# Optimization experiments

Measured on AMD Instinct MI355X. Metric: run time of the kernel, lower is better.

Reference implementation:

```python
import jax, jax.numpy as jnp
import numpy as np

B, N, F, H, HEADS = 2, 256, 64, 64, 4
C = HEADS * H  # n_coefficients (coefficients_mlp is Identity => must equal n_heads*hidden)
EPS = 1e-5
INF = 1e5


def _lin(key, fan_in, fan_out, bias=True):
    k1, k2 = jax.random.split(key)
    w = jax.random.normal(k1, (fan_in, fan_out), jnp.float32) * (1.0 / np.sqrt(fan_in))
    if bias:
        b = jax.random.normal(k2, (fan_out,), jnp.float32) * 0.01
        return w, b
    return w


def setup_inputs() -> dict:
    key = jax.random.key(0)
    ks = jax.random.split(key, 16)
    inp = dict(
        h=jax.random.normal(ks[0], (B, N, F), jnp.float32),
        x=jax.random.normal(ks[1], (B, N, 3), jnp.float32),
        v=jax.random.normal(ks[2], (B, N, 3), jnp.float32),
    )
    inp['edge_w1'], inp['edge_b1'] = _lin(ks[3], 2 * F + 1, H)
    inp['edge_w2'], inp['edge_b2'] = _lin(ks[4], H, H)
    inp['sem_w'], inp['sem_b'] = _lin(ks[5], H, HEADS)
    inp['post_w1'], inp['post_b1'] = _lin(ks[6], C, H)
    inp['post_w2'], inp['post_b2'] = _lin(ks[7], H, H)
    inp['node_w1'], inp['node_b1'] = _lin(ks[8], C + H + F, H)
    inp['node_w2'], inp['node_b2'] = _lin(ks[9], H, F)
    inp['vel_w1'], inp['vel_b1'] = _lin(ks[10], F, H)
    inp['vel_w2'] = _lin(ks[11], H, 1, bias=False) * 0.001  # xavier gain=0.001 analogue
    inp['vmix_w'] = _lin(ks[12], C, 1, bias=False)[:, 0]
    inp['log_gamma'] = -jnp.log(jnp.linspace(1.0, 5.0, HEADS)).astype(jnp.float32)
    return inp


def reference(h, x, v, edge_w1, edge_b1, edge_w2, edge_b2, sem_w, sem_b,
              post_w1, post_b1, post_w2, post_b2, node_w1, node_b1,
              node_w2, node_b2, vel_w1, vel_b1, vel_w2, vmix_w, log_gamma):
    silu = jax.nn.silu
    n = h.shape[-2]
    eye = jnp.eye(n, dtype=h.dtype)[:, :, None]  # [N,N,1] diagonal mask

    # pairwise geometry: entry [i,j] = x_j - x_i
    x_minus_xt = x[..., None, :, :] - x[..., :, None, :]                # [B,N,N,3]
    x_norm = jnp.sqrt((x_minus_xt ** 2).sum(-1, keepdims=True) + EPS)   # [B,N,N,1]

    # pairwise node-feature concat (h_j, h_i) + distance -> edge MLP
    h_j = jnp.broadcast_to(h[..., None, :, :], (B, n, n, F))
    h_i = jnp.broadcast_to(h[..., :, None, :], (B, n, n, F))
    h_cat = jnp.concatenate([h_j, h_i, x_norm], axis=-1)                # [B,N,N,2F+1]
    h_e_mtx = silu(silu(h_cat @ edge_w1 + edge_b1) @ edge_w2 + edge_b2)  # [B,N,N,H]

    # euclidean attention: softmin over j of gamma*dist, diagonal masked out
    dist = (x_norm + INF * eye) * jnp.exp(log_gamma)                    # [B,N,N,heads]
    euclid_att = jax.nn.softmax(-dist, axis=-2)
    # semantic attention: LeakyReLU(0.2) logits, diagonal masked, softmax over j
    sem = jax.nn.leaky_relu(h_e_mtx @ sem_w + sem_b, 0.2) - INF * eye
    sem_att = jax.nn.softmax(sem, axis=-2)
    comb_att = jax.nn.softmax(euclid_att * sem_att, axis=-2)            # [B,N,N,heads]

    # attention-weighted edge features, flattened over (H, heads)
    h_e_att = (h_e_mtx[..., :, None] * comb_att[..., None, :]).reshape(B, n, n, C)

    # spatial attention (coefficients_mlp is Identity)
    unit = x_minus_xt / (x_norm + EPS)                                  # [B,N,N,3]
    # combinations.mean(dim=-3) without materializing [B,N,N,C,3]
    comb_sum = jnp.einsum('bijc,bijd->bicd', h_e_att, unit) / n         # [B,N,C,3]
    comb_norm = (comb_sum ** 2).sum(-1)                                 # [B,N,C]
    h_comb = silu(silu(comb_norm @ post_w1 + post_b1) @ post_w2 + post_b2)

    # delta_v = mean_j (v_mixing over C of combinations)
    delta_v = jnp.einsum('bijc,c,bijd->bid', h_e_att, vmix_w, unit) / n  # [B,N,3]

    h_agg = h_e_att.sum(axis=-2)                                        # sum over j -> [B,N,C]
    out = jnp.concatenate([h, h_agg, h_comb], axis=-1)
    out = silu(silu(out @ node_w1 + node_b1) @ node_w2 + node_b2)
    h_new = h + out                                                     # residual

    # coordinate / velocity update
    v_scale = silu(h_new @ vel_w1 + vel_b1) @ vel_w2                    # [B,N,1]
    v_new = delta_v + v_scale * v
    x_new = x + v_new
    return h_new, x_new, v_new
```

## Files before the change

kernel.cpp:

```cpp
#include <hip/hip_runtime.h>
#include <hip/hip_bf16.h>
#include <math.h>

#define EPSV 1e-5f
#define INFV 1e5f

typedef short bf16x8 __attribute__((ext_vector_type(8)));
typedef float f32x4 __attribute__((ext_vector_type(4)));

__device__ __forceinline__ float rcp_f(float x) { return __builtin_amdgcn_rcpf(x); }
__device__ __forceinline__ float silu_f(float v) { return v * rcp_f(1.0f + __expf(-v)); }

__device__ __forceinline__ unsigned short f2bf(float f) {
  unsigned int u = __float_as_uint(f);
  u = (u + 0x7fffu + ((u >> 16) & 1u)) >> 16;
  return (unsigned short)u;
}
__device__ __forceinline__ float bf2f(unsigned short h) {
  return __uint_as_float(((unsigned int)h) << 16);
}
__device__ __forceinline__ unsigned int pkbf(float a, float b) {
  float2 f2; f2.x = a; f2.y = b;
  __hip_bfloat162 t = __float22bfloat162_rn(f2);
  unsigned int u;
  __builtin_memcpy(&u, &t, 4);
  return u;
}

__device__ __forceinline__ void gemm64(const unsigned short* A_lds, const unsigned short* B_lds,
                                       int w, int l15, int quad, f32x4 acc[4][4]) {
#pragma unroll
  for (int tr = 0; tr < 4; ++tr)
#pragma unroll
    for (int tc = 0; tc < 4; ++tc)
      acc[tr][tc] = (f32x4){0.f, 0.f, 0.f, 0.f};
#pragma unroll
  for (int ms = 0; ms < 64; ms += 32) {
    bf16x8 af[4], bfr[4];
#pragma unroll
    for (int tr = 0; tr < 4; ++tr)
      af[tr] = *reinterpret_cast<const bf16x8*>(&A_lds[(64 * w + 16 * tr + l15) * 72 + ms + quad * 8]);
#pragma unroll
    for (int tc = 0; tc < 4; ++tc)
      bfr[tc] = *reinterpret_cast<const bf16x8*>(&B_lds[(16 * tc + l15) * 72 + ms + quad * 8]);
#pragma unroll
    for (int tr = 0; tr < 4; ++tr)
#pragma unroll
      for (int tc = 0; tc < 4; ++tc)
        acc[tr][tc] = __builtin_amdgcn_mfma_f32_16x16x32_bf16(af[tr], bfr[tc], acc[tr][tc], 0, 0, 0);
  }
}

__global__ __launch_bounds__(256, 2) void k_all(
    const float* __restrict__ h, const float* __restrict__ x, const float* __restrict__ v,
    const float* __restrict__ ew1, const float* __restrict__ eb1,
    const float* __restrict__ ew2, const float* __restrict__ eb2,
    const float* __restrict__ semw, const float* __restrict__ semb,
    const float* __restrict__ pw1, const float* __restrict__ pb1,
    const float* __restrict__ pw2, const float* __restrict__ pb2,
    const float* __restrict__ nw1, const float* __restrict__ nb1,
    const float* __restrict__ nw2, const float* __restrict__ nb2,
    const float* __restrict__ vw1, const float* __restrict__ vb1,
    const float* __restrict__ vw2, const float* __restrict__ vmix,
    const float* __restrict__ lgam, float* __restrict__ out) {

  __shared__ __align__(16) unsigned short TH[256 * 72];
  __shared__ __align__(16) char R0[9216];
  __shared__ __align__(16) char R1[9216];
  __shared__ __align__(16) unsigned short E3T[16 * 72];
  __shared__ __align__(16) float4 unit_l[256];
  __shared__ float w1dk[64];
  __shared__ float eb1l[64];
  __shared__ __align__(16) float bms[256];

  const int bid = blockIdx.x;
  const int b   = bid >> 8;
  const int i   = bid & 255;
  const int bi  = bid;
  const int tid = threadIdx.x;
  const int j   = tid;
  const int bj  = (b << 8) | j;

  const int w    = tid >> 6;
  const int lid  = tid & 63;
  const int l15  = lid & 15;
  const int quad = lid >> 4;

  unsigned short* E2Ta = (unsigned short*)R0;
  unsigned short* E2Tb = (unsigned short*)R1;
  float*  sd    = (float*)R0;
  float4* cat_l = (float4*)R1;
  float*  cn_l  = (float*)(R1 + 4096);
  float*  hag_l = (float*)(R1 + 5120);
  float4* scS   = (float4*)bms;
  float4* scP   = (float4*)bms + 8;
  float4* scD   = (float4*)bms + 12;
  float*  dvs   = bms + 64;

  float warm = 0.f;
  {
#pragma unroll
    for (int q = 0; q < 4; ++q) warm += pw1[(4 * tid + q) * 16];
#pragma unroll
    for (int q = 0; q < 6; ++q) warm += nw1[(6 * tid + q) * 16];
    warm += pw2[tid * 16] + nw2[tid * 16] + vw1[tid * 16];
    if (tid < 64) warm += eb2[tid] + pb1[tid] + pb2[tid] + nb1[tid] +
                          nb2[tid] + vb1[tid] + vw2[tid];
  }

  const float xi0 = x[bi * 3 + 0], xi1 = x[bi * 3 + 1], xi2 = x[bi * 3 + 2];
  const float dx = x[bj * 3 + 0] - xi0;
  const float dy = x[bj * 3 + 1] - xi1;
  const float dz = x[bj * 3 + 2] - xi2;
  const float dn = sqrtf(dx * dx + dy * dy + dz * dz + EPSV);
  const float invn = rcp_f(dn + EPSV);
  const float ux = dx * invn, uy = dy * invn, uz = dz * invn;
  unit_l[j] = make_float4(ux, uy, uz, dn);

  {
    const float4* hb4 = reinterpret_cast<const float4*>(h + (size_t)(b << 8) * 64);
#pragma unroll
    for (int q = 0; q < 16; ++q) {
      int idx = q * 256 + tid;
      float4 f4 = hb4[idx];
      int row = idx >> 4, c4 = idx & 15;
      uint2 pk;
      pk.x = pkbf(f4.x, f4.y);
      pk.y = pkbf(f4.z, f4.w);
      *reinterpret_cast<uint2*>(&TH[row * 72 + c4 * 4]) = pk;
    }
  }
#pragma unroll
  for (int q = 0; q < 16; ++q) {
    int idx = q * 256 + tid;
    E2Ta[(idx & 63) * 72 + (idx >> 6)] = f2bf(ew1[idx]);
  }
#pragma unroll
  for (int q = 0; q < 16; ++q) {
    int idx = q * 256 + tid;
    E2Tb[(idx & 63) * 72 + (idx >> 6)] = f2bf(ew2[idx]);
  }
#pragma unroll
  for (int q = 0; q < 2; ++q) {
    int idx = q * 256 + tid;
    int n = idx >> 6, kk = idx & 63;
    E3T[n * 72 + kk] = f2bf((n < 4) ? semw[kk * 4 + n] : vmix[kk * 4 + (n - 4)]);
    E3T[(8 + n) * 72 + kk] = 0;
  }
  if (tid < 64) { w1dk[tid] = ew1[128 * 64 + tid]; eb1l[tid] = eb1[tid]; }
  {
    int s = tid >> 6, k = tid & 63;
    const float* hrow = h + (size_t)bi * 64;
    float bp = 0.f;
#pragma unroll
    for (int f2 = 0; f2 < 16; ++f2) {
      int f = s * 16 + f2;
      bp += hrow[f] * ew1[(64 + f) * 64 + k];
    }
    bms[s * 64 + k] = bp;
  }
  __syncthreads();

  f32x4 acc[4][4];
  gemm64(TH, E2Ta, w, l15, quad, acc);

#pragma unroll
  for (int tc = 0; tc < 4; ++tc) {
    int kc = 16 * tc + l15;
    float wd = w1dk[kc];
    float ak = eb1l[kc] + bms[kc] + bms[64 + kc] + bms[128 + kc] + bms[192 + kc];
#pragma unroll
    for (int tr = 0; tr < 4; ++tr)
#pragma unroll
      for (int r = 0; r < 4; ++r) {
        int row = 64 * w + 16 * tr + quad * 4 + r;
        TH[row * 72 + kc] = f2bf(silu_f(acc[tr][tc][r] + ak + unit_l[row].w * wd));
      }
  }
  __syncthreads();

  gemm64(TH, E2Tb, w, l15, quad, acc);
#pragma unroll
  for (int tc = 0; tc < 4; ++tc) {
    float b2 = eb2[16 * tc + l15];
#pragma unroll
    for (int tr = 0; tr < 4; ++tr)
#pragma unroll
      for (int r = 0; r < 4; ++r) {
        int row = 64 * w + 16 * tr + quad * 4 + r;
        TH[row * 72 + 16 * tc + l15] = f2bf(silu_f(acc[tr][tc][r] + b2));
      }
  }

  f32x4 acc3[4];
#pragma unroll
  for (int tr = 0; tr < 4; ++tr) acc3[tr] = (f32x4){0.f, 0.f, 0.f, 0.f};
#pragma unroll
  for (int ms = 0; ms < 64; ms += 32) {
    bf16x8 b3 = *reinterpret_cast<const bf16x8*>(&E3T[l15 * 72 + ms + quad * 8]);
#pragma unroll
    for (int tr = 0; tr < 4; ++tr) {
      bf16x8 a3 = *reinterpret_cast<const bf16x8*>(&TH[(64 * w + 16 * tr + l15) * 72 + ms + quad * 8]);
      acc3[tr] = __builtin_amdgcn_mfma_f32_16x16x32_bf16(a3, b3, acc3[tr], 0, 0, 0);
    }
  }
  if (l15 < 8) {
#pragma unroll
    for (int tr = 0; tr < 4; ++tr)
#pragma unroll
      for (int r = 0; r < 4; ++r)
        sd[(64 * w + 16 * tr + quad * 4 + r) * 8 + l15] = acc3[tr][r];
  }

  float4 s01 = *reinterpret_cast<const float4*>(sd + j * 8);
  float4 s23 = *reinterpret_cast<const float4*>(sd + j * 8 + 4);
  float4 sbv = *reinterpret_cast<const float4*>(semb);
  const float diag = (j == i) ? INFV : 0.0f;
  float4 sl;
  sl.x = s01.x + sbv.x; sl.y = s01.y + sbv.y; sl.z = s01.z + sbv.z; sl.w = s01.w + sbv.w;
  sl.x = ((sl.x > 0.f) ? sl.x : 0.2f * sl.x) - diag;
  sl.y = ((sl.y > 0.f) ? sl.y : 0.2f * sl.y) - diag;
  sl.z = ((sl.z > 0.f) ? sl.z : 0.2f * sl.z) - diag;
  sl.w = ((sl.w > 0.f) ? sl.w : 0.2f * sl.w) - diag;

  float4 lg4 = *reinterpret_cast<const float4*>(lgam);
  const float dni = dn + diag;
  float4 e_eu = make_float4(__expf(-dni * __expf(lg4.x)), __expf(-dni * __expf(lg4.y)),
                            __expf(-dni * __expf(lg4.z)), __expf(-dni * __expf(lg4.w)));
  float4 e_sem = make_float4(__expf(sl.x), __expf(sl.y), __expf(sl.z), __expf(sl.w));

  float4 a8 = e_eu, b8 = e_sem;
#pragma unroll
  for (int off = 32; off >= 1; off >>= 1) {
    a8.x += __shfl_xor(a8.x, off); a8.y += __shfl_xor(a8.y, off);
    a8.z += __shfl_xor(a8.z, off); a8.w += __shfl_xor(a8.w, off);
    b8.x += __shfl_xor(b8.x, off); b8.y += __shfl_xor(b8.y, off);
    b8.z += __shfl_xor(b8.z, off); b8.w += __shfl_xor(b8.w, off);
  }
  if (lid == 0) { scS[w] = a8; scS[4 + w] = b8; }
  __syncthreads();
  float4 Se, Ss;
  {
    float4 r0 = scS[0], r1 = scS[1], r2 = scS[2], r3 = scS[3];
    Se = make_float4(r0.x + r1.x + r2.x + r3.x, r0.y + r1.y + r2.y + r3.y,
                     r0.z + r1.z + r2.z + r3.z, r0.w + r1.w + r2.w + r3.w);
    float4 s0 = scS[4], s1 = scS[5], s2 = scS[6], s3 = scS[7];
    Ss = make_float4(s0.x + s1.x + s2.x + s3.x, s0.y + s1.y + s2.y + s3.y,
                     s0.z + s1.z + s2.z + s3.z, s0.w + s1.w + s2.w + s3.w);
  }

  float4 p = make_float4((e_eu.x * rcp_f(Se.x)) * (e_sem.x * rcp_f(Ss.x)),
                         (e_eu.y * rcp_f(Se.y)) * (e_sem.y * rcp_f(Ss.y)),
                         (e_eu.z * rcp_f(Se.z)) * (e_sem.z * rcp_f(Ss.z)),
                         (e_eu.w * rcp_f(Se.w)) * (e_sem.w * rcp_f(Ss.w)));
  float4 ep = make_float4(__expf(p.x), __expf(p.y), __expf(p.z), __expf(p.w));
  float4 sp8 = ep;
#pragma unroll
  for (int off = 32; off >= 1; off >>= 1) {
    sp8.x += __shfl_xor(sp8.x, off); sp8.y += __shfl_xor(sp8.y, off);
    sp8.z += __shfl_xor(sp8.z, off); sp8.w += __shfl_xor(sp8.w, off);
  }
  if (lid == 0) scP[w] = sp8;
  __syncthreads();
  float4 Sp;
  {
    float4 r0 = scP[0], r1 = scP[1], r2 = scP[2], r3 = scP[3];
    Sp = make_float4(r0.x + r1.x + r2.x + r3.x, r0.y + r1.y + r2.y + r3.y,
                     r0.z + r1.z + r2.z + r3.z, r0.w + r1.w + r2.w + r3.w);
  }
  float4 catt = make_float4(ep.x * rcp_f(Sp.x), ep.y * rcp_f(Sp.y),
                            ep.z * rcp_f(Sp.z), ep.w * rcp_f(Sp.w));
  cat_l[j] = catt;

  float s = catt.x * s23.x + catt.y * s23.y + catt.z * s23.z + catt.w * s23.w;
  float dvx = s * ux, dvy = s * uy, dvz = s * uz;
#pragma unroll
  for (int off = 32; off >= 1; off >>= 1) {
    dvx += __shfl_xor(dvx, off); dvy += __shfl_xor(dvy, off); dvz += __shfl_xor(dvz, off);
  }
  if (lid == 0) scD[w] = make_float4(dvx, dvy, dvz, 0.f);
  __syncthreads();
  if (j == 0) {
    float4 r0 = scD[0], r1 = scD[1], r2 = scD[2], r3 = scD[3];
    const float inv = 1.0f / 256.0f;
    dvs[0] = (r0.x + r1.x + r2.x + r3.x) * inv;
    dvs[1] = (r0.y + r1.y + r2.y + r3.y) * inv;
    dvs[2] = (r0.z + r1.z + r2.z + r3.z) * inv;
  }

  {
    const int jg   = lid >> 2;
    const int ksub = lid & 3;
    const int kb   = 16 * w + 4 * ksub;
    float agg[4][4], ax[4][4], ay[4][4], az[4][4];
#pragma unroll
    for (int kk = 0; kk < 4; ++kk)
#pragma unroll
      for (int hd = 0; hd < 4; ++hd) {
        agg[kk][hd] = 0.f; ax[kk][hd] = 0.f; ay[kk][hd] = 0.f; az[kk][hd] = 0.f;
      }
#pragma unroll 4
    for (int jr = 0; jr < 16; ++jr) {
      int jj = jr * 16 + jg;
      ushort4 hv4 = *reinterpret_cast<const ushort4*>(&TH[jj * 72 + kb]);
      float4 ca = cat_l[jj];
      float4 u  = unit_l[jj];
      float hev[4] = { bf2f(hv4.x), bf2f(hv4.y), bf2f(hv4.z), bf2f(hv4.w) };
#pragma unroll
      for (int kk = 0; kk < 4; ++kk) {
        float c0 = hev[kk] * ca.x, c1 = hev[kk] * ca.y, c2 = hev[kk] * ca.z, c3 = hev[kk] * ca.w;
        agg[kk][0] += c0; agg[kk][1] += c1; agg[kk][2] += c2; agg[kk][3] += c3;
        ax[kk][0] += c0 * u.x; ay[kk][0] += c0 * u.y; az[kk][0] += c0 * u.z;
        ax[kk][1] += c1 * u.x; ay[kk][1] += c1 * u.y; az[kk][1] += c1 * u.z;
        ax[kk][2] += c2 * u.x; ay[kk][2] += c2 * u.y; az[kk][2] += c2 * u.z;
        ax[kk][3] += c3 * u.x; ay[kk][3] += c3 * u.y; az[kk][3] += c3 * u.z;
      }
    }
#pragma unroll
    for (int off = 4; off <= 32; off <<= 1)
#pragma unroll
      for (int kk = 0; kk < 4; ++kk)
#pragma unroll
        for (int hd = 0; hd < 4; ++hd) {
          agg[kk][hd] += __shfl_xor(agg[kk][hd], off);
          ax[kk][hd]  += __shfl_xor(ax[kk][hd], off);
          ay[kk][hd]  += __shfl_xor(ay[kk][hd], off);
          az[kk][hd]  += __shfl_xor(az[kk][hd], off);
        }
    if (jg == 0) {
      const float inv = 1.0f / 256.0f;
#pragma unroll
      for (int kk = 0; kk < 4; ++kk) {
        int k = kb + kk;
        f32x4 cnv, hgv;
#pragma unroll
        for (int hd = 0; hd < 4; ++hd) {
          float cx = ax[kk][hd] * inv, cy = ay[kk][hd] * inv, cz = az[kk][hd] * inv;
          cnv[hd] = cx * cx + cy * cy + cz * cz;
          hgv[hd] = agg[kk][hd];
        }
        *reinterpret_cast<f32x4*>(&cn_l[k * 4])  = cnv;
        *reinterpret_cast<f32x4*>(&hag_l[k * 4]) = hgv;
      }
    }
  }
  __syncthreads();

  asm volatile("" :: "v"(warm));

  {
    const int k = lid;
    float* tmpg = (float*)TH;
    float a1 = 0.f;
#pragma unroll 16
    for (int m2 = 0; m2 < 64; ++m2) {
      int m = 64 * w + m2;
      a1 += cn_l[m] * pw1[m * 64 + k];
    }
    tmpg[w * 64 + k] = a1;
    if (w == 1 || w == 2) {
      float a2 = 0.f;
      int base = (w - 1) * 128;
#pragma unroll 16
      for (int m2 = 0; m2 < 128; ++m2) {
        int m = base + m2;
        a2 += hag_l[m] * nw1[(64 + m) * 64 + k];
      }
      tmpg[256 + (w - 1) * 64 + k] = a2;
    } else if (w == 3) {
      float a2 = 0.f;
      const float* hrow = h + (size_t)bi * 64;
#pragma unroll 16
      for (int m = 0; m < 64; ++m) a2 += hrow[m] * nw1[m * 64 + k];
      tmpg[384 + k] = a2;
    }
  }
  __syncthreads();

  if (w == 0) {
    const int k = lid;
    float* tmpg = (float*)TH;
    float* sh2  = tmpg + 512;

    float m1 = silu_f(pb1[k] + tmpg[k] + tmpg[64 + k] + tmpg[128 + k] + tmpg[192 + k]);
    sh2[k] = m1;

    float a = 0.f;
#pragma unroll 16
    for (int m = 0; m < 64; ++m) a += sh2[m] * pw2[m * 64 + k];
    float hcomb = silu_f(pb2[k] + a);
    sh2[64 + k] = hcomb;

    a = nb1[k] + tmpg[256 + k] + tmpg[320 + k] + tmpg[384 + k];
#pragma unroll 16
    for (int m = 0; m < 64; ++m) a += sh2[64 + m] * nw1[(320 + m) * 64 + k];
    sh2[128 + k] = silu_f(a);

    a = 0.f;
#pragma unroll 16
    for (int m = 0; m < 64; ++m) a += sh2[128 + m] * nw2[m * 64 + k];
    float hn = h[(size_t)bi * 64 + k] + silu_f(nb2[k] + a);
    out[(size_t)bi * 64 + k] = hn;
    sh2[192 + k] = hn;

    a = 0.f;
#pragma unroll 16
    for (int m = 0; m < 64; ++m) a += sh2[192 + m] * vw1[m * 64 + k];
    float vh = silu_f(vb1[k] + a) * vw2[k];
#pragma unroll
    for (int off = 32; off >= 1; off >>= 1) vh += __shfl_xor(vh, off);

    if (k == 0) {
      const float xi[3] = {xi0, xi1, xi2};
#pragma unroll
      for (int d = 0; d < 3; ++d) {
        float vn = dvs[d] + vh * v[bi * 3 + d];
        out[32768 + bi * 3 + d] = xi[d] + vn;
        out[34304 + bi * 3 + d] = vn;
      }
    }
  }
}

extern "C" void kernel_launch(void* const* d_in, const int* in_sizes, int n_in,
                              void* d_out, int out_size, void* d_ws, size_t ws_size,
                              hipStream_t stream) {
  const float* h    = (const float*)d_in[0];
  const float* x    = (const float*)d_in[1];
  const float* v    = (const float*)d_in[2];
  const float* ew1  = (const float*)d_in[3];
  const float* eb1  = (const float*)d_in[4];
  const float* ew2  = (const float*)d_in[5];
  const float* eb2  = (const float*)d_in[6];
  const float* semw = (const float*)d_in[7];
  const float* semb = (const float*)d_in[8];
  const float* pw1  = (const float*)d_in[9];
  const float* pb1  = (const float*)d_in[10];
  const float* pw2  = (const float*)d_in[11];
  const float* pb2  = (const float*)d_in[12];
  const float* nw1  = (const float*)d_in[13];
  const float* nb1  = (const float*)d_in[14];
  const float* nw2  = (const float*)d_in[15];
  const float* nb2  = (const float*)d_in[16];
  const float* vw1  = (const float*)d_in[17];
  const float* vb1  = (const float*)d_in[18];
  const float* vw2  = (const float*)d_in[19];
  const float* vmix = (const float*)d_in[20];
  const float* lgam = (const float*)d_in[21];
  float* out = (float*)d_out;

  k_all<<<512, 256, 0, stream>>>(h, x, v, ew1, eb1, ew2, eb2, semw, semb,
                                 pw1, pb1, pw2, pb2, nw1, nb1, nw2, nb2,
                                 vw1, vb1, vw2, vmix, lgam, out);
}
```

Measured before the change: 128.6 us.

## Pre-pack bf16 weights and h in prep kernel, load MFMA B fragments into registers

Result: no change. 130.0 us (+1.1%).

```diff
diff --git a/kernel.cpp b/kernel.cpp
--- a/kernel.cpp
+++ b/kernel.cpp
@@ -19,55 +19,50 @@
 __device__ __forceinline__ float bf2f(unsigned short h) {
   return __uint_as_float(((unsigned int)h) << 16);
 }
-__device__ __forceinline__ unsigned int pkbf(float a, float b) {
-  float2 f2; f2.x = a; f2.y = b;
-  __hip_bfloat162 t = __float22bfloat162_rn(f2);
-  unsigned int u;
-  __builtin_memcpy(&u, &t, 4);
-  return u;
+
+__global__ __launch_bounds__(256) void k_prep(
+    const float* __restrict__ ew1, const float* __restrict__ ew2,
+    const float* __restrict__ semw, const float* __restrict__ vmix,
+    const float* __restrict__ h, unsigned short* __restrict__ ws16) {
+  int gid = blockIdx.x * 256 + threadIdx.x;
+  if (gid < 4096) {
+    int fi = gid >> 9, l = (gid >> 3) & 63, e = gid & 7;
+    int tc = fi >> 1, ms = fi & 1;
+    int f = ms * 32 + (l >> 4) * 8 + e, k = tc * 16 + (l & 15);
+    ws16[gid] = f2bf(ew1[f * 64 + k]);
+  } else if (gid < 8192) {
+    int t = gid - 4096;
+    int fi = t >> 9, l = (t >> 3) & 63, e = t & 7;
+    int tc = fi >> 1, ms = fi & 1;
+    int f = ms * 32 + (l >> 4) * 8 + e, k = tc * 16 + (l & 15);
+    ws16[gid] = f2bf(ew2[f * 64 + k]);
+  } else if (gid < 9216) {
+    int t = gid - 8192;
+    int fi = t >> 9, l = (t >> 3) & 63, e = t & 7;
+    int n = l & 15, kk = fi * 32 + (l >> 4) * 8 + e;
+    float v = (n < 4) ? semw[kk * 4 + n] : (n < 8 ? vmix[kk * 4 + (n - 4)] : 0.f);
+    ws16[gid] = f2bf(v);
+  } else {
+    ws16[gid] = f2bf(h[gid - 9216]);
+  }
 }
 
-__device__ __forceinline__ void gemm64(const unsigned short* A_lds, const unsigned short* B_lds,
-                                       int w, int l15, int quad, f32x4 acc[4][4]) {
-#pragma unroll
-  for (int tr = 0; tr < 4; ++tr)
-#pragma unroll
-    for (int tc = 0; tc < 4; ++tc)
-      acc[tr][tc] = (f32x4){0.f, 0.f, 0.f, 0.f};
-#pragma unroll
-  for (int ms = 0; ms < 64; ms += 32) {
-    bf16x8 af[4], bfr[4];
-#pragma unroll
-    for (int tr = 0; tr < 4; ++tr)
-      af[tr] = *reinterpret_cast<const bf16x8*>(&A_lds[(64 * w + 16 * tr + l15) * 72 + ms + quad * 8]);
-#pragma unroll
-    for (int tc = 0; tc < 4; ++tc)
-      bfr[tc] = *reinterpret_cast<const bf16x8*>(&B_lds[(16 * tc + l15) * 72 + ms + quad * 8]);
-#pragma unroll
-    for (int tr = 0; tr < 4; ++tr)
-#pragma unroll
-      for (int tc = 0; tc < 4; ++tc)
-        acc[tr][tc] = __builtin_amdgcn_mfma_f32_16x16x32_bf16(af[tr], bfr[tc], acc[tr][tc], 0, 0, 0);
-  }
-}
-
-__global__ __launch_bounds__(256, 2) void k_all(
+__global__ __launch_bounds__(256, 3) void k_all(
     const float* __restrict__ h, const float* __restrict__ x, const float* __restrict__ v,
     const float* __restrict__ ew1, const float* __restrict__ eb1,
-    const float* __restrict__ ew2, const float* __restrict__ eb2,
-    const float* __restrict__ semw, const float* __restrict__ semb,
+    const float* __restrict__ eb2,
+    const float* __restrict__ semb,
     const float* __restrict__ pw1, const float* __restrict__ pb1,
     const float* __restrict__ pw2, const float* __restrict__ pb2,
     const float* __restrict__ nw1, const float* __restrict__ nb1,
     const float* __restrict__ nw2, const float* __restrict__ nb2,
     const float* __restrict__ vw1, const float* __restrict__ vb1,
-    const float* __restrict__ vw2, const float* __restrict__ vmix,
-    const float* __restrict__ lgam, float* __restrict__ out) {
+    const float* __restrict__ vw2,
+    const float* __restrict__ lgam,
+    const unsigned short* __restrict__ wsb, float* __restrict__ out) {
 
   __shared__ __align__(16) unsigned short TH[256 * 72];
-  __shared__ __align__(16) char R0[9216];
-  __shared__ __align__(16) char R1[9216];
-  __shared__ __align__(16) unsigned short E3T[16 * 72];
+  __shared__ __align__(16) float sd[2048];
   __shared__ __align__(16) float4 unit_l[256];
   __shared__ float w1dk[64];
   __shared__ float eb1l[64];
@@ -86,12 +81,9 @@
   const int l15  = lid & 15;
   const int quad = lid >> 4;
 
-  unsigned short* E2Ta = (unsigned short*)R0;
-  unsigned short* E2Tb = (unsigned short*)R1;
-  float*  sd    = (float*)R0;
-  float4* cat_l = (float4*)R1;
-  float*  cn_l  = (float*)(R1 + 4096);
-  float*  hag_l = (float*)(R1 + 5120);
+  float4* cat_l = (float4*)sd;
+  float*  cn_l  = sd + 1024;
+  float*  hag_l = sd + 1280;
   float4* scS   = (float4*)bms;
   float4* scP   = (float4*)bms + 8;
   float4* scD   = (float4*)bms + 12;
@@ -107,6 +99,11 @@
     if (tid < 64) warm += eb2[tid] + pb1[tid] + pb2[tid] + nb1[tid] +
                           nb2[tid] + vb1[tid] + vw2[tid];
   }
+
+  bf16x8 B1f[8];
+#pragma unroll
+  for (int fi = 0; fi < 8; ++fi)
+    B1f[fi] = *reinterpret_cast<const bf16x8*>(wsb + fi * 512 + lid * 8);
 
   const float xi0 = x[bi * 3 + 0], xi1 = x[bi * 3 + 1], xi2 = x[bi * 3 + 2];
   const float dx = x[bj * 3 + 0] - xi0;
@@ -117,35 +114,11 @@
   const float ux = dx * invn, uy = dy * invn, uz = dz * invn;
   unit_l[j] = make_float4(ux, uy, uz, dn);
 
-  {
-    const float4* hb4 = reinterpret_cast<const float4*>(h + (size_t)(b << 8) * 64);
-#pragma unroll
-    for (int q = 0; q < 16; ++q) {
-      int idx = q * 256 + tid;
-      float4 f4 = hb4[idx];
-      int row = idx >> 4, c4 = idx & 15;
-      uint2 pk;
-      pk.x = pkbf(f4.x, f4.y);
-      pk.y = pkbf(f4.z, f4.w);
-      *reinterpret_cast<uint2*>(&TH[row * 72 + c4 * 4]) = pk;
-    }
-  }
-#pragma unroll
-  for (int q = 0; q < 16; ++q) {
-    int idx = q * 256 + tid;
-    E2Ta[(idx & 63) * 72 + (idx >> 6)] = f2bf(ew1[idx]);
-  }
-#pragma unroll
-  for (int q = 0; q < 16; ++q) {
-    int idx = q * 256 + tid;
-    E2Tb[(idx & 63) * 72 + (idx >> 6)] = f2bf(ew2[idx]);
-  }
-#pragma unroll
-  for (int q = 0; q < 2; ++q) {
-    int idx = q * 256 + tid;
-    int n = idx >> 6, kk = idx & 63;
-    E3T[n * 72 + kk] = f2bf((n < 4) ? semw[kk * 4 + n] : vmix[kk * 4 + (n - 4)]);
-    E3T[(8 + n) * 72 + kk] = 0;
+#pragma unroll
+  for (int q = 0; q < 8; ++q) {
+    int c = q * 256 + tid;
+    bf16x8 hv = *reinterpret_cast<const bf16x8*>(wsb + 9216 + (b << 14) + c * 8);
+    *reinterpret_cast<bf16x8*>(&TH[(c >> 3) * 72 + (c & 7) * 8]) = hv;
   }
   if (tid < 64) { w1dk[tid] = ew1[128 * 64 + tid]; eb1l[tid] = eb1[tid]; }
   {
@@ -162,7 +135,23 @@
   __syncthreads();
 
   f32x4 acc[4][4];
-  gemm64(TH, E2Ta, w, l15, quad, acc);
+#pragma unroll
+  for (int tr = 0; tr < 4; ++tr)
+#pragma unroll
+    for (int tc = 0; tc < 4; ++tc)
+      acc[tr][tc] = (f32x4){0.f, 0.f, 0.f, 0.f};
+#pragma unroll
+  for (int ms = 0; ms < 2; ++ms) {
+    bf16x8 af[4];
+#pragma unroll
+    for (int tr = 0; tr < 4; ++tr)
+      af[tr] = *reinterpret_cast<const bf16x8*>(&TH[(64 * w + 16 * tr + l15) * 72 + ms * 32 + quad * 8]);
+#pragma unroll
+    for (int tr = 0; tr < 4; ++tr)
+#pragma unroll
+      for (int tc = 0; tc < 4; ++tc)
+        acc[tr][tc] = __builtin_amdgcn_mfma_f32_16x16x32_bf16(af[tr], B1f[tc * 2 + ms], acc[tr][tc], 0, 0, 0);
+  }
 
 #pragma unroll
   for (int tc = 0; tc < 4; ++tc) {
@@ -177,9 +166,33 @@
         TH[row * 72 + kc] = f2bf(silu_f(acc[tr][tc][r] + ak + unit_l[row].w * wd));
       }
   }
-  __syncthreads();
-
-  gemm64(TH, E2Tb, w, l15, quad, acc);
+  bf16x8 B2f[8];
+#pragma unroll
+  for (int fi = 0; fi < 8; ++fi)
+    B2f[fi] = *reinterpret_cast<const bf16x8*>(wsb + 4096 + fi * 512 + lid * 8);
+  __syncthreads();
+
+#pragma unroll
+  for (int tr = 0; tr < 4; ++tr)
+#pragma unroll
+    for (int tc = 0; tc < 4; ++tc)
+      acc[tr][tc] = (f32x4){0.f, 0.f, 0.f, 0.f};
+#pragma unroll
+  for (int ms = 0; ms < 2; ++ms) {
+    bf16x8 af[4];
+#pragma unroll
+    for (int tr = 0; tr < 4; ++tr)
+      af[tr] = *reinterpret_cast<const bf16x8*>(&TH[(64 * w + 16 * tr + l15) * 72 + ms * 32 + quad * 8]);
+#pragma unroll
+    for (int tr = 0; tr < 4; ++tr)
+#pragma unroll
+      for (int tc = 0; tc < 4; ++tc)
+        acc[tr][tc] = __builtin_amdgcn_mfma_f32_16x16x32_bf16(af[tr], B2f[tc * 2 + ms], acc[tr][tc], 0, 0, 0);
+  }
+  bf16x8 E3f[2];
+#pragma unroll
+  for (int fi = 0; fi < 2; ++fi)
+    E3f[fi] = *reinterpret_cast<const bf16x8*>(wsb + 8192 + fi * 512 + lid * 8);
 #pragma unroll
   for (int tc = 0; tc < 4; ++tc) {
     float b2 = eb2[16 * tc + l15];
@@ -196,12 +209,11 @@
 #pragma unroll
   for (int tr = 0; tr < 4; ++tr) acc3[tr] = (f32x4){0.f, 0.f, 0.f, 0.f};
 #pragma unroll
-  for (int ms = 0; ms < 64; ms += 32) {
-    bf16x8 b3 = *reinterpret_cast<const bf16x8*>(&E3T[l15 * 72 + ms + quad * 8]);
+  for (int ms = 0; ms < 2; ++ms) {
 #pragma unroll
     for (int tr = 0; tr < 4; ++tr) {
-      bf16x8 a3 = *reinterpret_cast<const bf16x8*>(&TH[(64 * w + 16 * tr + l15) * 72 + ms + quad * 8]);
-      acc3[tr] = __builtin_amdgcn_mfma_f32_16x16x32_bf16(a3, b3, acc3[tr], 0, 0, 0);
+      bf16x8 a3 = *reinterpret_cast<const bf16x8*>(&TH[(64 * w + 16 * tr + l15) * 72 + ms * 32 + quad * 8]);
+      acc3[tr] = __builtin_amdgcn_mfma_f32_16x16x32_bf16(a3, E3f[ms], acc3[tr], 0, 0, 0);
     }
   }
   if (l15 < 8) {
@@ -448,8 +460,10 @@
   const float* vmix = (const float*)d_in[20];
   const float* lgam = (const float*)d_in[21];
   float* out = (float*)d_out;
-
-  k_all<<<512, 256, 0, stream>>>(h, x, v, ew1, eb1, ew2, eb2, semw, semb,
+  unsigned short* ws16 = (unsigned short*)d_ws;
+
+  k_prep<<<164, 256, 0, stream>>>(ew1, ew2, semw, vmix, h, ws16);
+  k_all<<<512, 256, 0, stream>>>(h, x, v, ew1, eb1, eb2, semb,
                                  pw1, pb1, pw2, pb2, nw1, nb1, nw2, nb2,
-                                 vw1, vb1, vw2, vmix, lgam, out);
+                                 vw1, vb1, vw2, lgam, ws16, out);
 }
```
